# Kernel optimization log

Hardware: AMD Instinct MI355X
Metric: run time of the kernel (lower is better)

## Reference

```python
import jax, jax.numpy as jnp
import numpy as np

D_MODEL = 1024
D_STATE = 64
D_HEAD = 64
N_HEADS = 16
D_INNER = D_HEAD * N_HEADS  # 1024
K = 4  # conv kernel size
BATCH = 4
SEQ = 4096
LN_EPS = 1e-5


def setup_inputs() -> dict:
    key = jax.random.key(0)
    k0, k1, k2, k3, k4 = jax.random.split(key, 5)
    x = jax.random.normal(k0, (BATCH, SEQ, D_MODEL), jnp.float32)
    # nn.Linear(d_model, 2*d_inner + 2*d_state, bias=False): weight (out, in)
    in_proj_w = jax.random.normal(k1, (2 * D_INNER + 2 * D_STATE, D_MODEL), jnp.float32) / np.sqrt(D_MODEL).astype(np.float32)
    # depthwise Conv1d: weight (d_inner, 1, K), bias (d_inner,)
    conv_w = jax.random.normal(k2, (D_INNER, 1, K), jnp.float32) * 0.5
    conv_b = jax.random.normal(k3, (D_INNER,), jnp.float32) * 0.1
    # _init_parameters: A = -log(arange(1..d_state)) broadcast to (H, Dh, N)
    A_param = jnp.broadcast_to(-jnp.log(jnp.arange(1, D_STATE + 1, dtype=jnp.float32))[None, None, :],
                               (N_HEADS, D_HEAD, D_STATE))
    ln_w = jnp.ones((D_INNER,), jnp.float32)
    ln_b = jnp.zeros((D_INNER,), jnp.float32)
    out_proj_w = jax.random.normal(k4, (D_MODEL, D_INNER), jnp.float32) / np.sqrt(D_INNER).astype(np.float32)
    return {"x": x, "in_proj_w": in_proj_w, "conv_w": conv_w, "conv_b": conv_b,
            "A_param": A_param, "ln_w": ln_w, "ln_b": ln_b, "out_proj_w": out_proj_w}


def _ssd_scan(xh, Bm, Cm, A_param):
    # xh: (B, L, H, Dh); Bm, Cm: (B, L, N)
    A_disc = jnp.exp(-jnp.exp(A_param))  # (H, Dh, N)

    def step(h, inp):
        x_t, B_t, C_t = inp  # (B,H,Dh), (B,N), (B,N)
        h = h * A_disc + B_t[:, None, None, :] * x_t[..., None]  # (B,H,Dh,N)
        y_t = jnp.einsum('bhdn,bn->bhd', h, C_t)
        return h, y_t

    b = xh.shape[0]
    h0 = jnp.zeros((b, N_HEADS, D_HEAD, D_STATE), xh.dtype)
    xs = (jnp.swapaxes(xh, 0, 1), jnp.swapaxes(Bm, 0, 1), jnp.swapaxes(Cm, 0, 1))
    _, ys = jax.lax.scan(step, h0, xs)  # ys: (L, B, H, Dh)
    return jnp.swapaxes(ys, 0, 1)  # (B, L, H, Dh)


def reference(x, in_proj_w, conv_w, conv_b, A_param, ln_w, ln_b, out_proj_w):
    b, L, _ = x.shape
    xBC = x @ in_proj_w.T  # (B, L, 2*d_inner + 2*d_state)
    xc = xBC[..., :D_INNER]
    z = xBC[..., D_INNER:2 * D_INNER]
    Bm = xBC[..., 2 * D_INNER:2 * D_INNER + D_STATE]
    Cm = xBC[..., 2 * D_INNER + D_STATE:]
    # causal depthwise conv (padding=3 then truncate == left-pad K-1)
    xt = jnp.swapaxes(xc, 1, 2)  # (B, C, L)
    y = jax.lax.conv_general_dilated(xt, conv_w, window_strides=(1,), padding=[(K - 1, 0)],
                                     feature_group_count=D_INNER,
                                     dimension_numbers=('NCH', 'OIH', 'NCH'))
    xc = jnp.swapaxes(y + conv_b[None, :, None], 1, 2)  # (B, L, d_inner)
    xc = jax.nn.silu(xc)
    xh = xc.reshape(b, L, N_HEADS, D_HEAD)
    yssd = _ssd_scan(xh, Bm, Cm, A_param).reshape(b, L, D_INNER)
    yg = yssd * jax.nn.silu(z)
    mu = yg.mean(-1, keepdims=True)
    var = yg.var(-1, keepdims=True)
    yn = (yg - mu) / jnp.sqrt(var + LN_EPS) * ln_w + ln_b
    return yn @ out_proj_w.T
```

## Files before the change

### kernel.cpp

```cpp
#include <hip/hip_runtime.h>

typedef unsigned short u16;
typedef unsigned int u32;
typedef __attribute__((ext_vector_type(8))) short bf16x8;
typedef __attribute__((ext_vector_type(4))) float f32x4;

#define BATCH 4
#define SEQ 4096
#define DMODEL 1024
#define DINNER 1024
#define NPROJ 2176
#define MROWS (BATCH*SEQ)
#define NCHUNK 64
#define CLEN 64
#define NPAD 2304

__device__ __forceinline__ float bf2f(u16 u) {
    union { u32 i; float f; } v; v.i = ((u32)u) << 16; return v.f;
}
__device__ __forceinline__ u16 f2bf(float f) {
    union { float f; u32 i; } v; v.f = f;
    u32 r = v.i + 0x7FFFu + ((v.i >> 16) & 1u);
    return (u16)(r >> 16);
}
__device__ __forceinline__ float silu_f(float x) { return x / (1.0f + expf(-x)); }

__device__ __forceinline__ void gload8f(const u16* p, float* o) {
    bf16x8 v = *(const bf16x8*)p;
    #pragma unroll
    for (int j = 0; j < 8; ++j) o[j] = bf2f((u16)v[j]);
}

__device__ __forceinline__ void ld_lds16(const u16* g, u16* l) {
    __builtin_amdgcn_global_load_lds(
        (const __attribute__((address_space(1))) u32*)g,
        (__attribute__((address_space(3))) u32*)l, 16, 0, 0);
}

__global__ __launch_bounds__(256) void cast_f2b(
    const float* __restrict__ src, u16* __restrict__ dst, int n8)
{
    int i = blockIdx.x * 256 + threadIdx.x;
    if (i >= n8) return;
    size_t o = (size_t)i * 8;
    float4 a = *(const float4*)(src + o);
    float4 b = *(const float4*)(src + o + 4);
    u16 v[8] = {f2bf(a.x), f2bf(a.y), f2bf(a.z), f2bf(a.w),
                f2bf(b.x), f2bf(b.y), f2bf(b.z), f2bf(b.w)};
    *(bf16x8*)(dst + o) = *(bf16x8*)v;
}

__global__ __launch_bounds__(256) void cast_w1p_k(
    const float* __restrict__ src, u16* __restrict__ dst)
{
    int i = blockIdx.x * 256 + threadIdx.x;
    int row = i >> 7;
    size_t o = (size_t)i * 8;
    u16 v[8];
    if (row < NPROJ) {
        float4 a = *(const float4*)(src + o);
        float4 b = *(const float4*)(src + o + 4);
        v[0]=f2bf(a.x); v[1]=f2bf(a.y); v[2]=f2bf(a.z); v[3]=f2bf(a.w);
        v[4]=f2bf(b.x); v[5]=f2bf(b.y); v[6]=f2bf(b.z); v[7]=f2bf(b.w);
    } else {
        #pragma unroll
        for (int j = 0; j < 8; ++j) v[j] = 0;
    }
    *(bf16x8*)(dst + o) = *(bf16x8*)v;
}

__global__ __launch_bounds__(256) void tables_k(
    const float* __restrict__ A_param, float* __restrict__ l2a_g,
    float* __restrict__ apw, float* __restrict__ ainv)
{
    __shared__ float l2s[64];
    int tid = threadIdx.x;
    if (tid < 64) {
        float v = -expf(A_param[tid]) * 1.44269504088896340736f;
        l2s[tid] = v;
        l2a_g[tid] = v;
    }
    __syncthreads();
    #pragma unroll
    for (int i = 0; i < 16; ++i) {
        int e = tid * 16 + i;
        int t = e >> 6, n = e & 63;
        float x = (float)t * l2s[n];
        apw[e]  = exp2f(x);
        ainv[e] = exp2f(-x);
    }
}

#define GK 1024
#define GNT 16

template<typename TO, int GN, int NV, int LDC>
__global__ __launch_bounds__(512, 2) void gemm8p_k(
    const u16* __restrict__ A, const u16* __restrict__ B, TO* __restrict__ C)
{
    __shared__ u16 lds[65536];

    const int cpx = (GN * 64) >> 3;
    const int bid = blockIdx.x;
    const int swz = (bid & 7) * cpx + (bid >> 3);
    const int bm = swz / GN, bn = swz % GN;
    const int m0 = bm * 256, n0 = bn * 256;

    const int tid = threadIdx.x;
    const int wid = tid >> 6, lane = tid & 63;
    const int wm = wid >> 2, wn = wid & 3;
    const int quad = lane >> 4, l16 = lane & 15;
    const int xsw = (l16 & 7) << 3;

    u16* L = lds;
    const u16* Ab = A + (size_t)m0 * GK;
    const u16* Bb = B + (size_t)n0 * GK;

    auto stage = [&](const u16* gbase, u16* ldsb) {
        {
            int c = tid;
            int row = c >> 3, slot = (c & 7) ^ (row & 7);
            ld_lds16(gbase + (size_t)row * GK + slot * 8,
                     ldsb + ((tid & ~63) << 3));
        }
        {
            int c = 512 + tid;
            int row = c >> 3, slot = (c & 7) ^ (row & 7);
            ld_lds16(gbase + (size_t)row * GK + slot * 8,
                     ldsb + ((512 + (tid & ~63)) << 3));
        }
    };
    auto rdfrag = [&](const u16* base, int rh, int kh) -> bf16x8 {
        return *(const bf16x8*)(base + rh * 64 + ((kh * 32 + quad * 8) ^ xsw));
    };

    bf16x8 aLo[4][2], aHi[4][2], bLo[2][2], bHi[2][2];
    f32x4 acc[8][4] = {};

    stage(Ab,                     L);
    stage(Ab + 128 * GK,          L + 8192);
    stage(Bb,                     L + 32768);
    stage(Bb + 128 * GK,          L + 40960);
    stage(Ab + 64,                L + 16384);
    stage(Ab + 128 * GK + 64,     L + 24576);
    asm volatile("s_waitcnt vmcnt(4)" ::: "memory");
    __builtin_amdgcn_s_barrier();
    {
        const u16* Ard = L + wm * 8192;
        #pragma unroll
        for (int i = 0; i < 4; ++i)
            #pragma unroll
            for (int kh = 0; kh < 2; ++kh)
                aLo[i][kh] = rdfrag(Ard, i * 16 + l16, kh);
    }

    for (int t = 0; t < GNT; ++t) {
        const int cb = t & 1;
        u16* Acur = L + cb * 16384;
        u16* Anxt = L + (cb ^ 1) * 16384;
        u16* Bnxt = L + 32768 + (cb ^ 1) * 16384;
        const u16* ArdC = Acur + wm * 8192;
        const u16* ArdN = Anxt + wm * 8192;
        const u16* BrdC = L + 32768 + cb * 16384 + (wn >> 1) * 8192;
        const int brh = (wn & 1) * 64;

        #pragma unroll
        for (int j = 0; j < 2; ++j)
            #pragma unroll
            for (int kh = 0; kh < 2; ++kh)
                bLo[j][kh] = rdfrag(BrdC, brh + j * 16 + l16, kh);
        if (t + 1 < GNT) stage(Bb + (t + 1) * 64, Bnxt);
        __builtin_amdgcn_s_barrier();
        asm volatile("s_waitcnt lgkmcnt(0)" ::: "memory");
        __builtin_amdgcn_s_setprio(1);
        #pragma unroll
        for (int kh = 0; kh < 2; ++kh)
            #pragma unroll
            for (int i = 0; i < 4; ++i)
                #pragma unroll
                for (int j = 0; j < 2; ++j)
                    acc[i][j] = __builtin_amdgcn_mfma_f32_16x16x32_bf16(
                        aLo[i][kh], bLo[j][kh], acc[i][j], 0, 0, 0);
        __builtin_amdgcn_s_setprio(0);
        __builtin_amdgcn_s_barrier();

        #pragma unroll
        for (int j = 0; j < 2; ++j)
            #pragma unroll
            for (int kh = 0; kh < 2; ++kh)
                bHi[j][kh] = rdfrag(BrdC, brh + 32 + j * 16 + l16, kh);
        if (t + 1 < GNT) stage(Bb + 128 * GK + (t + 1) * 64, Bnxt + 8192);
        __builtin_amdgcn_s_barrier();
        asm volatile("s_waitcnt lgkmcnt(0)" ::: "memory");
        __builtin_amdgcn_s_setprio(1);
        #pragma unroll
        for (int kh = 0; kh < 2; ++kh)
            #pragma unroll
            for (int i = 0; i < 4; ++i)
                #pragma unroll
                for (int j = 0; j < 2; ++j)
                    acc[i][2 + j] = __builtin_amdgcn_mfma_f32_16x16x32_bf16(
                        aLo[i][kh], bHi[j][kh], acc[i][2 + j], 0, 0, 0);
        __builtin_amdgcn_s_setprio(0);
        __builtin_amdgcn_s_barrier();

        #pragma unroll
        for (int i = 0; i < 4; ++i)
            #pragma unroll
            for (int kh = 0; kh < 2; ++kh)
                aHi[i][kh] = rdfrag(ArdC, 64 + i * 16 + l16, kh);
        if (t + 2 < GNT) stage(Ab + (t + 2) * 64, Acur);
        if (t + 2 < GNT)      { asm volatile("s_waitcnt vmcnt(6)" ::: "memory"); }
        else if (t + 1 < GNT) { asm volatile("s_waitcnt vmcnt(4)" ::: "memory"); }
        __builtin_amdgcn_s_barrier();
        asm volatile("s_waitcnt lgkmcnt(0)" ::: "memory");
        __builtin_amdgcn_s_setprio(1);
        #pragma unroll
        for (int kh = 0; kh < 2; ++kh)
            #pragma unroll
            for (int i = 0; i < 4; ++i)
                #pragma unroll
                for (int j = 0; j < 2; ++j)
                    acc[4 + i][2 + j] = __builtin_amdgcn_mfma_f32_16x16x32_bf16(
                        aHi[i][kh], bHi[j][kh], acc[4 + i][2 + j], 0, 0, 0);
        __builtin_amdgcn_s_setprio(0);
        __builtin_amdgcn_s_barrier();

        if (t + 1 < GNT) {
            #pragma unroll
            for (int i = 0; i < 4; ++i)
                #pragma unroll
                for (int kh = 0; kh < 2; ++kh)
                    aLo[i][kh] = rdfrag(ArdN, i * 16 + l16, kh);
        }
        if (t + 2 < GNT) stage(Ab + 128 * GK + (t + 2) * 64, Acur + 8192);
        if (t + 2 < GNT)      { asm volatile("s_waitcnt vmcnt(4)" ::: "memory"); }
        else if (t + 1 < GNT) { asm volatile("s_waitcnt vmcnt(0)" ::: "memory"); }
        __builtin_amdgcn_s_barrier();
        asm volatile("s_waitcnt lgkmcnt(0)" ::: "memory");
        __builtin_amdgcn_s_setprio(1);
        #pragma unroll
        for (int kh = 0; kh < 2; ++kh)
            #pragma unroll
            for (int i = 0; i < 4; ++i)
                #pragma unroll
                for (int j = 0; j < 2; ++j)
                    acc[4 + i][j] = __builtin_amdgcn_mfma_f32_16x16x32_bf16(
                        aHi[i][kh], bLo[j][kh], acc[4 + i][j], 0, 0, 0);
        __builtin_amdgcn_s_setprio(0);
        __builtin_amdgcn_s_barrier();
    }

    __syncthreads();
    if constexpr (sizeof(TO) == 2) {
        u16* eld = lds;
        #pragma unroll
        for (int i = 0; i < 8; ++i)
            #pragma unroll
            for (int j = 0; j < 4; ++j)
                #pragma unroll
                for (int r = 0; r < 4; ++r)
                    eld[(size_t)(wm * 128 + i * 16 + quad * 4 + r) * 256 +
                        wn * 64 + j * 16 + l16] = f2bf(acc[i][j][r]);
        __syncthreads();
        #pragma unroll
        for (int rep = 0; rep < 16; ++rep) {
            int cc = rep * 512 + tid;
            int row = cc >> 5, c8 = (cc & 31) * 8;
            if (n0 + c8 < NV)
                *(bf16x8*)(C + (size_t)(m0 + row) * LDC + n0 + c8) =
                    *(const bf16x8*)(eld + (size_t)row * 256 + c8);
        }
    } else {
        float* eldf = (float*)lds;
        #pragma unroll
        for (int h = 0; h < 2; ++h) {
            if (wm == h) {
                #pragma unroll
                for (int i = 0; i < 8; ++i)
                    #pragma unroll
                    for (int j = 0; j < 4; ++j)
                        #pragma unroll
                        for (int r = 0; r < 4; ++r)
                            eldf[(size_t)(i * 16 + quad * 4 + r) * 256 +
                                 wn * 64 + j * 16 + l16] = acc[i][j][r];
            }
            __syncthreads();
            #pragma unroll
            for (int rep = 0; rep < 16; ++rep) {
                int cc = rep * 512 + tid;
                int row = cc >> 6, c4 = (cc & 63) * 4;
                *(float4*)(C + (size_t)(m0 + h * 128 + row) * LDC + n0 + c4) =
                    *(const float4*)(eldf + (size_t)row * 256 + c4);
            }
            __syncthreads();
        }
    }
}

#define CRPT 8
__global__ __launch_bounds__(256) void conv_k(
    const u16* __restrict__ xBC, const float* __restrict__ conv_w,
    const float* __restrict__ conv_b, u16* __restrict__ xact)
{
    int o = blockIdx.x * 256 + threadIdx.x;
    int c0 = (o & 127) * 8;
    int rg = o >> 7;
    int row0 = rg * CRPT;
    int l0 = row0 & (SEQ - 1);

    float4 wv[8];
    #pragma unroll
    for (int j = 0; j < 8; ++j)
        wv[j] = *(const float4*)(conv_w + (c0 + j) * 4);
    float bias[8];
    {
        float4 b0 = *(const float4*)(conv_b + c0);
        float4 b1 = *(const float4*)(conv_b + c0 + 4);
        bias[0]=b0.x; bias[1]=b0.y; bias[2]=b0.z; bias[3]=b0.w;
        bias[4]=b1.x; bias[5]=b1.y; bias[6]=b1.z; bias[7]=b1.w;
    }

    float win[3][8];
    #pragma unroll
    for (int k = 0; k < 3; ++k) {
        if (l0 - 3 + k < 0) {
            #pragma unroll
            for (int j = 0; j < 8; ++j) win[k][j] = 0.f;
        } else {
            gload8f(xBC + (size_t)(row0 - 3 + k) * NPROJ + c0, win[k]);
        }
    }
    #pragma unroll
    for (int r = 0; r < CRPT; ++r) {
        float cur[8];
        gload8f(xBC + (size_t)(row0 + r) * NPROJ + c0, cur);
        u16 outv[8];
        #pragma unroll
        for (int j = 0; j < 8; ++j) {
            float acc = bias[j]
                + win[0][j] * wv[j].x + win[1][j] * wv[j].y
                + win[2][j] * wv[j].z + cur[j]    * wv[j].w;
            outv[j] = f2bf(silu_f(acc));
        }
        *(bf16x8*)(xact + (size_t)(row0 + r) * DINNER + c0) = *(bf16x8*)outv;
        #pragma unroll
        for (int j = 0; j < 8; ++j) {
            win[0][j] = win[1][j]; win[1][j] = win[2][j]; win[2][j] = cur[j];
        }
    }
}

__global__ __launch_bounds__(256) void ssd_intra_k(
    const u16* __restrict__ xact, u16* __restrict__ xBC,
    u16* __restrict__ Sh, const float* __restrict__ apw,
    const float* __restrict__ ainv)
{
    __shared__ u16 Pl[64][72];
    __shared__ u16 Ql[64][72];
    __shared__ u16 Gl[64][72];
    __shared__ u16 Qt[64][72];
    __shared__ u16 Xt[64][72];

    const int dg = blockIdx.x, c = blockIdx.y, b = blockIdx.z;
    const int dcol = dg * 64;
    const int l0 = c * CLEN;
    const int tid = threadIdx.x;
    const int w = tid >> 6, lane = tid & 63;
    const int quad = lane >> 4, l16 = lane & 15;
    const int tstrip = 16 * w;

    {
        const int st_t = tid >> 3, st_n8 = (tid & 7) * 8;
        #pragma unroll
        for (int rep = 0; rep < 2; ++rep) {
            int t = rep * 32 + st_t;
            size_t row = (size_t)(b * SEQ + l0 + t) * NPROJ;
            float Bv[8], Cv[8];
            gload8f(xBC + row + 2048 + st_n8, Bv);
            gload8f(xBC + row + 2112 + st_n8, Cv);
            float4 aw0 = *(const float4*)&apw[t * 64 + st_n8];
            float4 aw1 = *(const float4*)&apw[t * 64 + st_n8 + 4];
            float4 ai0 = *(const float4*)&ainv[t * 64 + st_n8];
            float4 ai1 = *(const float4*)&ainv[t * 64 + st_n8 + 4];
            float4 ar0 = *(const float4*)&apw[(63 - t) * 64 + st_n8];
            float4 ar1 = *(const float4*)&apw[(63 - t) * 64 + st_n8 + 4];
            float aw[8] = {aw0.x,aw0.y,aw0.z,aw0.w,aw1.x,aw1.y,aw1.z,aw1.w};
            float ai[8] = {ai0.x,ai0.y,ai0.z,ai0.w,ai1.x,ai1.y,ai1.z,ai1.w};
            float ar[8] = {ar0.x,ar0.y,ar0.z,ar0.w,ar1.x,ar1.y,ar1.z,ar1.w};
            u16 p8[8], q8[8];
            #pragma unroll
            for (int j = 0; j < 8; ++j) {
                p8[j] = f2bf(Cv[j] * aw[j]);
                q8[j] = f2bf(Bv[j] * ai[j]);
            }
            *(bf16x8*)&Pl[t][st_n8] = *(bf16x8*)p8;
            *(bf16x8*)&Ql[t][st_n8] = *(bf16x8*)q8;
            #pragma unroll
            for (int j = 0; j < 8; ++j)
                Qt[st_n8 + j][t] = f2bf(Bv[j] * ar[j]);
        }
    }
    {
        #pragma unroll
        for (int rep = 0; rep < 2; ++rep) {
            int idx = rep * 256 + tid;
            int xt_t = idx >> 3, xt_d8 = (idx & 7) * 8;
            float xv[8];
            gload8f(xact + (size_t)(b * SEQ + l0 + xt_t) * DINNER + dcol + xt_d8, xv);
            #pragma unroll
            for (int j = 0; j < 8; ++j) Xt[xt_d8 + j][xt_t] = f2bf(xv[j]);
        }
    }
    __syncthreads();

    bf16x8 af0 = *(const bf16x8*)&Pl[tstrip + l16][0  + quad * 8];
    bf16x8 af1 = *(const bf16x8*)&Pl[tstrip + l16][32 + quad * 8];
    f32x4 g[4] = {};
    #pragma unroll
    for (int j4 = 0; j4 < 4; ++j4) {
        bf16x8 b0 = *(const bf16x8*)&Ql[j4 * 16 + l16][0  + quad * 8];
        bf16x8 b1 = *(const bf16x8*)&Ql[j4 * 16 + l16][32 + quad * 8];
        g[j4] = __builtin_amdgcn_mfma_f32_16x16x32_bf16(af0, b0, g[j4], 0, 0, 0);
        g[j4] = __builtin_amdgcn_mfma_f32_16x16x32_bf16(af1, b1, g[j4], 0, 0, 0);
    }
    __syncthreads();

    #pragma unroll
    for (int j4 = 0; j4 < 4; ++j4) {
        #pragma unroll
        for (int r = 0; r < 4; ++r) {
            int t = tstrip + quad * 4 + r;
            int s = j4 * 16 + l16;
            float val = (s <= t) ? g[j4][r] : 0.f;
            u16 hi = f2bf(val);
            Ql[t][s] = hi;
            Gl[t][s] = f2bf(val - bf2f(hi));
        }
    }
    __syncthreads();

    bf16x8 gh0 = *(const bf16x8*)&Ql[tstrip + l16][0  + quad * 8];
    bf16x8 gh1 = *(const bf16x8*)&Ql[tstrip + l16][32 + quad * 8];
    bf16x8 gl0 = *(const bf16x8*)&Gl[tstrip + l16][0  + quad * 8];
    bf16x8 gl1 = *(const bf16x8*)&Gl[tstrip + l16][32 + quad * 8];
    bf16x8 qt0 = *(const bf16x8*)&Qt[tstrip + l16][0  + quad * 8];
    bf16x8 qt1 = *(const bf16x8*)&Qt[tstrip + l16][32 + quad * 8];

    #pragma unroll
    for (int dt = 0; dt < 4; ++dt) {
        bf16x8 x0 = *(const bf16x8*)&Xt[dt * 16 + l16][0  + quad * 8];
        bf16x8 x1 = *(const bf16x8*)&Xt[dt * 16 + l16][32 + quad * 8];
        f32x4 y = {};
        y = __builtin_amdgcn_mfma_f32_16x16x32_bf16(gh0, x0, y, 0, 0, 0);
        y = __builtin_amdgcn_mfma_f32_16x16x32_bf16(gh1, x1, y, 0, 0, 0);
        y = __builtin_amdgcn_mfma_f32_16x16x32_bf16(gl0, x0, y, 0, 0, 0);
        y = __builtin_amdgcn_mfma_f32_16x16x32_bf16(gl1, x1, y, 0, 0, 0);
        f32x4 s4 = {};
        s4 = __builtin_amdgcn_mfma_f32_16x16x32_bf16(qt0, x0, s4, 0, 0, 0);
        s4 = __builtin_amdgcn_mfma_f32_16x16x32_bf16(qt1, x1, s4, 0, 0, 0);
        #pragma unroll
        for (int r = 0; r < 4; ++r) {
            int t = tstrip + quad * 4 + r;
            xBC[(size_t)(b * SEQ + l0 + t) * NPROJ + dcol + dt * 16 + l16] = f2bf(y[r]);
            int n = tstrip + quad * 4 + r;
            Sh[((size_t)((b * NCHUNK + c) * 64 + n)) * 1024 + dcol + dt * 16 + l16] = f2bf(s4[r]);
        }
    }
}

__global__ __launch_bounds__(256) void state_scan_k(
    u16* __restrict__ Sh, const float* __restrict__ l2a)
{
    int gid = blockIdx.x * 256 + threadIdx.x;
    int b = gid >> 16, r = gid & 65535, n = r >> 10;
    float a64 = exp2f(64.f * l2a[n]);
    float v = 0.f;
    size_t base = ((size_t)b << 22) + r;
    for (int c = 0; c < NCHUNK; ++c) {
        size_t addr = base + ((size_t)c << 16);
        float s = bf2f(Sh[addr]);
        Sh[addr] = f2bf(v);
        v = fmaf(v, a64, s);
    }
}

__global__ __launch_bounds__(256) void ssd_inter_k(
    u16* __restrict__ xBC, const u16* __restrict__ Sh,
    const float* __restrict__ apw, const float* __restrict__ l2a)
{
    __shared__ u16 Pl[64][72];
    __shared__ u16 Vt[64][72];

    const int dg = blockIdx.x, c = blockIdx.y, b = blockIdx.z;
    const int dcol = dg * 64;
    const int l0 = c * CLEN;
    const int tid = threadIdx.x;
    const int w = tid >> 6, lane = tid & 63;
    const int quad = lane >> 4, l16 = lane & 15;
    const int tstrip = 16 * w;

    {
        const int st_t = tid >> 3, st_n8 = (tid & 7) * 8;
        #pragma unroll
        for (int rep = 0; rep < 2; ++rep) {
            int t = rep * 32 + st_t;
            float Cv[8];
            gload8f(xBC + (size_t)(b * SEQ + l0 + t) * NPROJ + 2112 + st_n8, Cv);
            float4 aw0 = *(const float4*)&apw[t * 64 + st_n8];
            float4 aw1 = *(const float4*)&apw[t * 64 + st_n8 + 4];
            float aw[8] = {aw0.x,aw0.y,aw0.z,aw0.w,aw1.x,aw1.y,aw1.z,aw1.w};
            u16 p8[8];
            #pragma unroll
            for (int j = 0; j < 8; ++j) p8[j] = f2bf(Cv[j] * aw[j]);
            *(bf16x8*)&Pl[t][st_n8] = *(bf16x8*)p8;
        }
    }
    {
        #pragma unroll
        for (int rep = 0; rep < 2; ++rep) {
            int idx = rep * 256 + tid;
            int vn = idx >> 3, vd8 = (idx & 7) * 8;
            float an = exp2f(l2a[vn]);
            bf16x8 vv = *(const bf16x8*)&Sh[((size_t)((b * NCHUNK + c) * 64 + vn)) * 1024 + dcol + vd8];
            #pragma unroll
            for (int j = 0; j < 8; ++j) Vt[vd8 + j][vn] = f2bf(an * bf2f((u16)vv[j]));
        }
    }
    __syncthreads();

    bf16x8 af0 = *(const bf16x8*)&Pl[tstrip + l16][0  + quad * 8];
    bf16x8 af1 = *(const bf16x8*)&Pl[tstrip + l16][32 + quad * 8];
    #pragma unroll
    for (int dt = 0; dt < 4; ++dt) {
        bf16x8 hb0 = *(const bf16x8*)&Vt[dt * 16 + l16][0  + quad * 8];
        bf16x8 hb1 = *(const bf16x8*)&Vt[dt * 16 + l16][32 + quad * 8];
        f32x4 y = {};
        y = __builtin_amdgcn_mfma_f32_16x16x32_bf16(af0, hb0, y, 0, 0, 0);
        y = __builtin_amdgcn_mfma_f32_16x16x32_bf16(af1, hb1, y, 0, 0, 0);
        #pragma unroll
        for (int r = 0; r < 4; ++r) {
            int t = tstrip + quad * 4 + r;
            size_t addr = (size_t)(b * SEQ + l0 + t) * NPROJ + dcol + dt * 16 + l16;
            xBC[addr] = f2bf(bf2f(xBC[addr]) + y[r]);
        }
    }
}

__global__ __launch_bounds__(256) void gate_k(
    const u16* __restrict__ xBC, const float* __restrict__ ln_w,
    const float* __restrict__ ln_b, u16* __restrict__ yn)
{
    __shared__ float r1[4], r2[4];
    const int row = blockIdx.x;
    const int tid = threadIdx.x;
    const int lane = tid & 63, wid = tid >> 6;
    const size_t base = (size_t)row * NPROJ;

    float gv[4];
    {
        const ushort4 yv = *(const ushort4*)(xBC + base + tid * 4);
        const ushort4 zv = *(const ushort4*)(xBC + base + 1024 + tid * 4);
        gv[0] = bf2f(yv.x) * silu_f(bf2f(zv.x));
        gv[1] = bf2f(yv.y) * silu_f(bf2f(zv.y));
        gv[2] = bf2f(yv.z) * silu_f(bf2f(zv.z));
        gv[3] = bf2f(yv.w) * silu_f(bf2f(zv.w));
    }
    float ps = gv[0] + gv[1] + gv[2] + gv[3];
    float pq = gv[0]*gv[0] + gv[1]*gv[1] + gv[2]*gv[2] + gv[3]*gv[3];
    #pragma unroll
    for (int off = 1; off < 64; off <<= 1) {
        ps += __shfl_xor(ps, off);
        pq += __shfl_xor(pq, off);
    }
    if (lane == 0) { r1[wid] = ps; r2[wid] = pq; }
    __syncthreads();
    float ts = r1[0] + r1[1] + r1[2] + r1[3];
    float tq = r2[0] + r2[1] + r2[2] + r2[3];
    float mu = ts * (1.0f / DINNER);
    float var = tq * (1.0f / DINNER) - mu * mu;
    float inv = rsqrtf(var + 1e-5f);

    u16 outv[4];
    #pragma unroll
    for (int j = 0; j < 4; ++j) {
        int c = tid * 4 + j;
        float v = (gv[j] - mu) * inv * ln_w[c] + ln_b[c];
        outv[j] = f2bf(v);
    }
    *(ushort4*)(yn + (size_t)row * DINNER + tid * 4) = *(ushort4*)outv;
}

extern "C" void kernel_launch(void* const* d_in, const int* in_sizes, int n_in,
                              void* d_out, int out_size, void* d_ws, size_t ws_size,
                              hipStream_t stream) {
    const float* x   = (const float*)d_in[0];
    const float* w1  = (const float*)d_in[1];
    const float* cw  = (const float*)d_in[2];
    const float* cb  = (const float*)d_in[3];
    const float* ap  = (const float*)d_in[4];
    const float* lnw = (const float*)d_in[5];
    const float* lnb = (const float*)d_in[6];
    const float* w2  = (const float*)d_in[7];
    float* out = (float*)d_out;

    u16* xBC   = (u16*)d_ws;
    u16* xact  = xBC + (size_t)MROWS * NPROJ;
    u16* x_bf  = xact;
    u16* w2_bf = xact + (size_t)MROWS * DINNER;
    float* l2a  = (float*)(w2_bf + (size_t)DMODEL * DINNER);
    float* apw  = l2a + 64;
    float* ainv = apw + 4096;
    u16* w1p = (u16*)d_out;
    u16* Sh  = (u16*)d_out;

    cast_f2b<<<(MROWS * DMODEL / 8) / 256, 256, 0, stream>>>(x, x_bf, MROWS * DMODEL / 8);
    cast_w1p_k<<<(NPAD * DMODEL / 8) / 256, 256, 0, stream>>>(w1, w1p);
    cast_f2b<<<(DMODEL * DINNER / 8) / 256, 256, 0, stream>>>(w2, w2_bf, DMODEL * DINNER / 8);
    tables_k<<<1, 256, 0, stream>>>(ap, l2a, apw, ainv);

    gemm8p_k<u16, 9, NPROJ, NPROJ><<<9 * 64, 512, 0, stream>>>(x_bf, w1p, xBC);
    conv_k<<<(MROWS / CRPT * 128) / 256, 256, 0, stream>>>(xBC, cw, cb, xact);

    ssd_intra_k<<<dim3(16, NCHUNK, BATCH), 256, 0, stream>>>(xact, xBC, Sh, apw, ainv);
    state_scan_k<<<1024, 256, 0, stream>>>(Sh, l2a);
    ssd_inter_k<<<dim3(16, NCHUNK, BATCH), 256, 0, stream>>>(xBC, Sh, apw, l2a);

    gate_k<<<MROWS, 256, 0, stream>>>(xBC, lnw, lnb, xact);
    gemm8p_k<float, 4, DMODEL, DMODEL><<<4 * 64, 512, 0, stream>>>(xact, w2_bf, out);
}
```

Before: 372.4 us.

## Fuse causal depthwise conv into SSD intra-chunk kernel and relax GEMM launch bounds

```diff
diff --git a/kernel.cpp b/kernel.cpp
--- a/kernel.cpp
+++ b/kernel.cpp
@@ -95,7 +95,7 @@
 #define GNT 16
 
 template<typename TO, int GN, int NV, int LDC>
-__global__ __launch_bounds__(512, 2) void gemm8p_k(
+__global__ __launch_bounds__(512, 1) void gemm8p_k(
     const u16* __restrict__ A, const u16* __restrict__ B, TO* __restrict__ C)
 {
     __shared__ u16 lds[65536];
@@ -298,61 +298,9 @@
     }
 }
 
-#define CRPT 8
-__global__ __launch_bounds__(256) void conv_k(
-    const u16* __restrict__ xBC, const float* __restrict__ conv_w,
-    const float* __restrict__ conv_b, u16* __restrict__ xact)
-{
-    int o = blockIdx.x * 256 + threadIdx.x;
-    int c0 = (o & 127) * 8;
-    int rg = o >> 7;
-    int row0 = rg * CRPT;
-    int l0 = row0 & (SEQ - 1);
-
-    float4 wv[8];
-    #pragma unroll
-    for (int j = 0; j < 8; ++j)
-        wv[j] = *(const float4*)(conv_w + (c0 + j) * 4);
-    float bias[8];
-    {
-        float4 b0 = *(const float4*)(conv_b + c0);
-        float4 b1 = *(const float4*)(conv_b + c0 + 4);
-        bias[0]=b0.x; bias[1]=b0.y; bias[2]=b0.z; bias[3]=b0.w;
-        bias[4]=b1.x; bias[5]=b1.y; bias[6]=b1.z; bias[7]=b1.w;
-    }
-
-    float win[3][8];
-    #pragma unroll
-    for (int k = 0; k < 3; ++k) {
-        if (l0 - 3 + k < 0) {
-            #pragma unroll
-            for (int j = 0; j < 8; ++j) win[k][j] = 0.f;
-        } else {
-            gload8f(xBC + (size_t)(row0 - 3 + k) * NPROJ + c0, win[k]);
-        }
-    }
-    #pragma unroll
-    for (int r = 0; r < CRPT; ++r) {
-        float cur[8];
-        gload8f(xBC + (size_t)(row0 + r) * NPROJ + c0, cur);
-        u16 outv[8];
-        #pragma unroll
-        for (int j = 0; j < 8; ++j) {
-            float acc = bias[j]
-                + win[0][j] * wv[j].x + win[1][j] * wv[j].y
-                + win[2][j] * wv[j].z + cur[j]    * wv[j].w;
-            outv[j] = f2bf(silu_f(acc));
-        }
-        *(bf16x8*)(xact + (size_t)(row0 + r) * DINNER + c0) = *(bf16x8*)outv;
-        #pragma unroll
-        for (int j = 0; j < 8; ++j) {
-            win[0][j] = win[1][j]; win[1][j] = win[2][j]; win[2][j] = cur[j];
-        }
-    }
-}
-
 __global__ __launch_bounds__(256) void ssd_intra_k(
-    const u16* __restrict__ xact, u16* __restrict__ xBC,
+    const float* __restrict__ conv_w, const float* __restrict__ conv_b,
+    const u16* __restrict__ xBC, u16* __restrict__ yout,
     u16* __restrict__ Sh, const float* __restrict__ apw,
     const float* __restrict__ ainv)
 {
@@ -402,14 +350,40 @@
         }
     }
     {
+        const int xt_d8 = (tid & 7) * 8;
+        const int ch0 = dcol + xt_d8;
+        float4 wv[8];
+        #pragma unroll
+        for (int j = 0; j < 8; ++j)
+            wv[j] = *(const float4*)(conv_w + (ch0 + j) * 4);
+        float bias[8];
+        {
+            float4 b0 = *(const float4*)(conv_b + ch0);
+            float4 b1 = *(const float4*)(conv_b + ch0 + 4);
+            bias[0]=b0.x; bias[1]=b0.y; bias[2]=b0.z; bias[3]=b0.w;
+            bias[4]=b1.x; bias[5]=b1.y; bias[6]=b1.z; bias[7]=b1.w;
+        }
         #pragma unroll
         for (int rep = 0; rep < 2; ++rep) {
-            int idx = rep * 256 + tid;
-            int xt_t = idx >> 3, xt_d8 = (idx & 7) * 8;
-            float xv[8];
-            gload8f(xact + (size_t)(b * SEQ + l0 + xt_t) * DINNER + dcol + xt_d8, xv);
-            #pragma unroll
-            for (int j = 0; j < 8; ++j) Xt[xt_d8 + j][xt_t] = f2bf(xv[j]);
+            int xt_t = (tid >> 3) + rep * 32;
+            float acc[8];
+            #pragma unroll
+            for (int j = 0; j < 8; ++j) acc[j] = bias[j];
+            #pragma unroll
+            for (int k = 0; k < 4; ++k) {
+                int lt = l0 + xt_t - 3 + k;
+                if (lt < 0) continue;
+                float v[8];
+                gload8f(xBC + (size_t)(b * SEQ + lt) * NPROJ + ch0, v);
+                #pragma unroll
+                for (int j = 0; j < 8; ++j) {
+                    const float* wj = (const float*)&wv[j];
+                    acc[j] += v[j] * wj[k];
+                }
+            }
+            #pragma unroll
+            for (int j = 0; j < 8; ++j)
+                Xt[xt_d8 + j][xt_t] = f2bf(silu_f(acc[j]));
         }
     }
     __syncthreads();
@@ -462,7 +436,7 @@
         #pragma unroll
         for (int r = 0; r < 4; ++r) {
             int t = tstrip + quad * 4 + r;
-            xBC[(size_t)(b * SEQ + l0 + t) * NPROJ + dcol + dt * 16 + l16] = f2bf(y[r]);
+            yout[(size_t)(b * SEQ + l0 + t) * DINNER + dcol + dt * 16 + l16] = f2bf(y[r]);
             int n = tstrip + quad * 4 + r;
             Sh[((size_t)((b * NCHUNK + c) * 64 + n)) * 1024 + dcol + dt * 16 + l16] = f2bf(s4[r]);
         }
@@ -486,8 +460,9 @@
 }
 
 __global__ __launch_bounds__(256) void ssd_inter_k(
-    u16* __restrict__ xBC, const u16* __restrict__ Sh,
-    const float* __restrict__ apw, const float* __restrict__ l2a)
+    u16* __restrict__ Y, const u16* __restrict__ xBC,
+    const u16* __restrict__ Sh, const float* __restrict__ apw,
+    const float* __restrict__ l2a)
 {
     __shared__ u16 Pl[64][72];
     __shared__ u16 Vt[64][72];
@@ -541,26 +516,26 @@
         #pragma unroll
         for (int r = 0; r < 4; ++r) {
             int t = tstrip + quad * 4 + r;
-            size_t addr = (size_t)(b * SEQ + l0 + t) * NPROJ + dcol + dt * 16 + l16;
-            xBC[addr] = f2bf(bf2f(xBC[addr]) + y[r]);
+            size_t addr = (size_t)(b * SEQ + l0 + t) * DINNER + dcol + dt * 16 + l16;
+            Y[addr] = f2bf(bf2f(Y[addr]) + y[r]);
         }
     }
 }
 
 __global__ __launch_bounds__(256) void gate_k(
-    const u16* __restrict__ xBC, const float* __restrict__ ln_w,
-    const float* __restrict__ ln_b, u16* __restrict__ yn)
+    const u16* __restrict__ Y, const u16* __restrict__ xBC,
+    const float* __restrict__ ln_w, const float* __restrict__ ln_b,
+    u16* __restrict__ yn)
 {
     __shared__ float r1[4], r2[4];
     const int row = blockIdx.x;
     const int tid = threadIdx.x;
     const int lane = tid & 63, wid = tid >> 6;
-    const size_t base = (size_t)row * NPROJ;
 
     float gv[4];
     {
-        const ushort4 yv = *(const ushort4*)(xBC + base + tid * 4);
-        const ushort4 zv = *(const ushort4*)(xBC + base + 1024 + tid * 4);
+        const ushort4 yv = *(const ushort4*)(Y + (size_t)row * DINNER + tid * 4);
+        const ushort4 zv = *(const ushort4*)(xBC + (size_t)row * NPROJ + 1024 + tid * 4);
         gv[0] = bf2f(yv.x) * silu_f(bf2f(zv.x));
         gv[1] = bf2f(yv.y) * silu_f(bf2f(zv.y));
         gv[2] = bf2f(yv.z) * silu_f(bf2f(zv.z));
@@ -620,12 +595,11 @@
     tables_k<<<1, 256, 0, stream>>>(ap, l2a, apw, ainv);
 
     gemm8p_k<u16, 9, NPROJ, NPROJ><<<9 * 64, 512, 0, stream>>>(x_bf, w1p, xBC);
-    conv_k<<<(MROWS / CRPT * 128) / 256, 256, 0, stream>>>(xBC, cw, cb, xact);
-
-    ssd_intra_k<<<dim3(16, NCHUNK, BATCH), 256, 0, stream>>>(xact, xBC, Sh, apw, ainv);
+
+    ssd_intra_k<<<dim3(16, NCHUNK, BATCH), 256, 0, stream>>>(cw, cb, xBC, xact, Sh, apw, ainv);
     state_scan_k<<<1024, 256, 0, stream>>>(Sh, l2a);
-    ssd_inter_k<<<dim3(16, NCHUNK, BATCH), 256, 0, stream>>>(xBC, Sh, apw, l2a);
-
-    gate_k<<<MROWS, 256, 0, stream>>>(xBC, lnw, lnb, xact);
+    ssd_inter_k<<<dim3(16, NCHUNK, BATCH), 256, 0, stream>>>(xact, xBC, Sh, apw, l2a);
+
+    gate_k<<<MROWS, 256, 0, stream>>>(xact, xBC, lnw, lnb, xact);
     gemm8p_k<float, 4, DMODEL, DMODEL><<<4 * 64, 512, 0, stream>>>(xact, w2_bf, out);
 }
```

Result: slower. 383.6 us, median of 3 (+3.0%).
